# Kernel tuning notes

Measured on AMD Instinct MI355X. Metric: run time of the kernel, lower is better.

The kernel has to match this reference:

```python
import jax, jax.numpy as jnp
import numpy as np

K = 2  # top-k experts per token


def setup_inputs() -> dict:
    key = jax.random.key(0)
    ks = jax.random.split(key, 5)
    N, D, F, E = 8192, 1024, 1024, 8
    s = lambda d: 1.0 / np.sqrt(d)
    return {
        "x": jax.random.normal(ks[0], (N, D), jnp.float32),
        "Wr": jax.random.normal(ks[1], (D, E), jnp.float32) * s(D),
        "br": jax.random.normal(ks[2], (E,), jnp.float32) * 0.01,
        "We": jax.random.normal(ks[3], (E, D, F), jnp.float32) * s(D),
        "be": jax.random.normal(ks[4], (E, F), jnp.float32) * 0.01,
    }


def reference(x, Wr, br, We, be):
    # Router: logits [N, E] -> top-k -> softmax over the k selected logits
    logits = x @ Wr + br
    topv, idx = jax.lax.top_k(logits, K)            # [N, K]
    w = jax.nn.softmax(topv, axis=-1)               # [N, K]
    # All-expert dense compute (eval mode: dropout is identity)
    h = jnp.einsum("nd,edf->nef", x, We) + be       # [N, E, F]
    h = jax.nn.gelu(h, approximate=False)           # exact GELU (torch nn.GELU default)
    # Gather the k selected experts per token and combine
    sel = jnp.take_along_axis(h, idx[:, :, None], axis=1)  # [N, K, F]
    out = jnp.einsum("nk,nkf->nf", w, sel)          # [N, F]
    return out
```

## Files before the change

### kernel.cpp

```cpp
#include <hip/hip_runtime.h>
#include <hip/hip_bf16.h>
#include <math.h>
#include <stdint.h>

#define N_TOK 8192
#define DIM   1024
#define FDIM  1024
#define NEXP  8

typedef unsigned short u16;
typedef __bf16 bf16x8 __attribute__((ext_vector_type(8)));
typedef float  f32x4  __attribute__((ext_vector_type(4)));

__device__ __forceinline__ u16 f2bf(float f) {
  union { float f; uint32_t u; } v; v.f = f;
  return (u16)((v.u + 0x7fffu + ((v.u >> 16) & 1u)) >> 16);
}

__global__ __launch_bounds__(256) void k_prep(
    const float* __restrict__ x, const float* __restrict__ Wr,
    const float* __restrict__ br, const float* __restrict__ We,
    u16* __restrict__ xb, u16* __restrict__ WeT,
    int* __restrict__ topk_idx, float* __restrict__ topk_w0) {
  __shared__ float tile[64][65];
  int b = blockIdx.x;
  if (b < 2048) {
    int n = b * 4 + (threadIdx.x >> 6);
    int lane = threadIdx.x & 63;
    const float4* xr = (const float4*)(x + (size_t)n * DIM);
    ushort4* xbr = (ushort4*)(xb + (size_t)n * DIM);
    double acc[8];
#pragma unroll
    for (int e = 0; e < 8; ++e) acc[e] = 0.0;
#pragma unroll
    for (int i = 0; i < 4; ++i) {
      int d4 = lane + 64 * i;
      float4 v = xr[d4];
      ushort4 o;
      o.x = f2bf(v.x); o.y = f2bf(v.y); o.z = f2bf(v.z); o.w = f2bf(v.w);
      xbr[d4] = o;
      float vv[4] = {v.x, v.y, v.z, v.w};
      const float* wr = Wr + (size_t)d4 * 4 * NEXP;
#pragma unroll
      for (int j = 0; j < 4; ++j) {
        float4 w0 = *(const float4*)(wr + j * 8);
        float4 w1 = *(const float4*)(wr + j * 8 + 4);
        acc[0] += (double)vv[j] * w0.x; acc[1] += (double)vv[j] * w0.y;
        acc[2] += (double)vv[j] * w0.z; acc[3] += (double)vv[j] * w0.w;
        acc[4] += (double)vv[j] * w1.x; acc[5] += (double)vv[j] * w1.y;
        acc[6] += (double)vv[j] * w1.z; acc[7] += (double)vv[j] * w1.w;
      }
    }
#pragma unroll
    for (int e = 0; e < 8; ++e) {
      for (int off = 32; off; off >>= 1) acc[e] += __shfl_xor(acc[e], off);
    }
    if (lane == 0) {
      double lg[8];
#pragma unroll
      for (int e = 0; e < 8; ++e) lg[e] = acc[e] + (double)br[e];
      int i0 = 0; double v0 = lg[0];
#pragma unroll
      for (int e = 1; e < 8; ++e) if (lg[e] > v0) { v0 = lg[e]; i0 = e; }
      int i1 = -1; double v1 = -1e300;
#pragma unroll
      for (int e = 0; e < 8; ++e) if (e != i0 && lg[e] > v1) { v1 = lg[e]; i1 = e; }
      float w0 = 1.0f / (1.0f + expf((float)(v1 - v0)));
      topk_idx[n] = i0 | (i1 << 8);
      topk_w0[n] = w0;
    }
  } else {
    int tb = b - 2048;
    int e = tb >> 8;
    int d0 = ((tb >> 4) & 15) * 64, f0 = (tb & 15) * 64;
    int t = threadIdx.x;
    int lr = t >> 6, lc = t & 63;
    const float* src = We + (size_t)e * DIM * FDIM + (size_t)d0 * FDIM + f0;
#pragma unroll
    for (int i = 0; i < 16; ++i)
      tile[i * 4 + lr][lc] = src[(size_t)(i * 4 + lr) * FDIM + lc];
    __syncthreads();
    u16* dst = WeT + (size_t)e * FDIM * DIM + (size_t)f0 * DIM + d0;
#pragma unroll
    for (int i = 0; i < 16; ++i)
      dst[(size_t)(i * 4 + lr) * DIM + lc] = f2bf(tile[lc][i * 4 + lr]);
  }
}

__global__ __launch_bounds__(256) void k_build_lists(const int* __restrict__ topk_idx,
                                                     int* __restrict__ gcount,
                                                     int* __restrict__ token_list) {
  __shared__ int lcount[8];
  __shared__ int lbase[8];
  int t = threadIdx.x;
  int n = blockIdx.x * 256 + t;
  if (t < 8) lcount[t] = 0;
  __syncthreads();
  int pk = topk_idx[n];
  int e0 = pk & 0xff, e1 = (pk >> 8) & 0xff;
  int p0 = atomicAdd(&lcount[e0], 1);
  int p1 = atomicAdd(&lcount[e1], 1);
  __syncthreads();
  if (t < 8) lbase[t] = atomicAdd(&gcount[t], lcount[t]);
  __syncthreads();
  token_list[e0 * N_TOK + lbase[e0] + p0] = n * 2;
  token_list[e1 * N_TOK + lbase[e1] + p1] = n * 2 + 1;
}

#define BM 128
#define BN 128
#define BK 64
#define NWG 1088

__global__ __launch_bounds__(256, 2) void k_moe_gemm(
    const u16* __restrict__ xb, const u16* __restrict__ WeT,
    const int* __restrict__ gcount, const int* __restrict__ token_list,
    u16* __restrict__ hbuf) {
  int b = blockIdx.x;
  int w = (b & 7) * (NWG / 8) + (b >> 3);
  int e = -1, my = 0, fx = 0, cnt = 0, pfx = 0;
#pragma unroll
  for (int i = 0; i < NEXP; ++i) {
    int c = gcount[i];
    int tiles = ((c + BM - 1) >> 7) * (FDIM / BN);
    if (e < 0 && w < pfx + tiles) {
      e = i; int lw = w - pfx; my = lw >> 3; fx = lw & 7; cnt = c;
    }
    pfx += tiles;
  }
  if (e < 0) return;
  int m0 = my * BM, f0 = fx * BN;

  __shared__ u16 sA[BM * BK];
  __shared__ u16 sB[BN * BK];

  int tid = threadIdx.x;
  int lane = tid & 63, wid = tid >> 6;
  int wm = wid >> 1, wn = wid & 1;
  int rA = lane & 15, kg = lane >> 4;

  const int* tl = token_list + e * N_TOK;

  const u16* aA[4];
  const u16* aB[4];
  int cnt1 = cnt - 1;
#pragma unroll
  for (int it = 0; it < 4; ++it) {
    int c = it * 256 + tid;
    int row = c >> 3, cj = c & 7;
    int sw = (cj * 8) ^ ((row & 7) << 3);
    int slot = m0 + row; if (slot > cnt1) slot = cnt1;
    int tok = tl[slot] >> 1;
    aA[it] = xb + (size_t)tok * DIM + sw;
    aB[it] = WeT + ((size_t)(e * FDIM + f0 + row)) * DIM + sw;
  }

  f32x4 zero = {0.f, 0.f, 0.f, 0.f};
  f32x4 acc[4][4];
#pragma unroll
  for (int mi = 0; mi < 4; ++mi)
#pragma unroll
    for (int ni = 0; ni < 4; ++ni) acc[mi][ni] = zero;

  const char* pA = (const char*)sA + (wm * 64 + rA) * 128;
  const char* pB = (const char*)sB + (wn * 64 + rA) * 128;
  int swz = (rA & 7) << 4;

  for (int kt = 0; kt < DIM / BK; ++kt) {
    int k0 = kt * BK;
#pragma unroll
    for (int it = 0; it < 4; ++it) {
      __builtin_amdgcn_global_load_lds(
          (const __attribute__((address_space(1))) void*)(aA[it] + k0),
          (__attribute__((address_space(3))) void*)(sA + (it * 256 + tid) * 8), 16, 0, 0);
      __builtin_amdgcn_global_load_lds(
          (const __attribute__((address_space(1))) void*)(aB[it] + k0),
          (__attribute__((address_space(3))) void*)(sB + (it * 256 + tid) * 8), 16, 0, 0);
    }
    __syncthreads();
#pragma unroll
    for (int kk = 0; kk < 2; ++kk) {
      int kb = ((kk << 6) | (kg << 4)) ^ swz;
      bf16x8 av[4], bv[4];
#pragma unroll
      for (int mi = 0; mi < 4; ++mi)
        av[mi] = *(const bf16x8*)(pA + mi * 2048 + kb);
#pragma unroll
      for (int ni = 0; ni < 4; ++ni)
        bv[ni] = *(const bf16x8*)(pB + ni * 2048 + kb);
#pragma unroll
      for (int mi = 0; mi < 4; ++mi)
#pragma unroll
        for (int ni = 0; ni < 4; ++ni)
          acc[mi][ni] = __builtin_amdgcn_mfma_f32_16x16x32_bf16(av[mi], bv[ni], acc[mi][ni], 0, 0, 0);
    }
    __syncthreads();
  }

#pragma unroll
  for (int mi = 0; mi < 4; ++mi) {
#pragma unroll
    for (int j = 0; j < 4; ++j) {
      int slot = m0 + wm * 64 + mi * 16 + kg * 4 + j;
      if (slot < cnt) {
        int tok2 = tl[slot];
        u16* hrow = hbuf + (size_t)tok2 * FDIM;
        int colf = f0 + wn * 64 + rA;
#pragma unroll
        for (int ni = 0; ni < 4; ++ni)
          hrow[colf + ni * 16] = f2bf(acc[mi][ni][j]);
      }
    }
  }
}

__global__ __launch_bounds__(256) void k_combine(const u16* __restrict__ hbuf,
                                                 const int* __restrict__ topk_idx,
                                                 const float* __restrict__ topk_w0,
                                                 const float* __restrict__ be,
                                                 float* __restrict__ out) {
  int n = blockIdx.x * 2 + (threadIdx.x >> 7);
  int t = threadIdx.x & 127;
  int pk = topk_idx[n];
  int e0 = pk & 0xff, e1 = (pk >> 8) & 0xff;
  float w0 = topk_w0[n], w1 = 1.0f - w0;
  const bf16x8* r0 = (const bf16x8*)(hbuf + (size_t)(2 * n) * FDIM);
  const bf16x8* r1 = (const bf16x8*)(hbuf + (size_t)(2 * n + 1) * FDIM);
  bf16x8 a = r0[t], c = r1[t];
  const float* b0 = be + e0 * FDIM + t * 8;
  const float* b1 = be + e1 * FDIM + t * 8;
  float4 b0a = *(const float4*)(b0), b0b = *(const float4*)(b0 + 4);
  float4 b1a = *(const float4*)(b1), b1b = *(const float4*)(b1 + 4);
  float bb0[8] = {b0a.x, b0a.y, b0a.z, b0a.w, b0b.x, b0b.y, b0b.z, b0b.w};
  float bb1[8] = {b1a.x, b1a.y, b1a.z, b1a.w, b1b.x, b1b.y, b1b.z, b1b.w};
  float o[8];
#pragma unroll
  for (int i = 0; i < 8; ++i) {
    float v0 = (float)a[i] + bb0[i];
    float v1 = (float)c[i] + bb1[i];
    float g0 = 0.5f * v0 * (1.0f + erff(v0 * 0.70710678118654752f));
    float g1 = 0.5f * v1 * (1.0f + erff(v1 * 0.70710678118654752f));
    o[i] = w0 * g0 + w1 * g1;
  }
  float* orow = out + (size_t)n * FDIM + t * 8;
  *(float4*)(orow)     = *(float4*)(o);
  *(float4*)(orow + 4) = *(float4*)(o + 4);
}

extern "C" void kernel_launch(void* const* d_in, const int* in_sizes, int n_in,
                              void* d_out, int out_size, void* d_ws, size_t ws_size,
                              hipStream_t stream) {
  const float* x  = (const float*)d_in[0];
  const float* Wr = (const float*)d_in[1];
  const float* br = (const float*)d_in[2];
  const float* We = (const float*)d_in[3];
  const float* be = (const float*)d_in[4];
  float* out = (float*)d_out;

  char* ws = (char*)d_ws;
  u16* xb = (u16*)ws;                ws += (size_t)N_TOK * DIM * 2;
  u16* WeT = (u16*)ws;               ws += (size_t)NEXP * FDIM * DIM * 2;
  u16* hbuf = (u16*)ws;              ws += (size_t)2 * N_TOK * FDIM * 2;
  int* token_list = (int*)ws;        ws += (size_t)NEXP * N_TOK * 4;
  int* topk_idx = (int*)ws;          ws += (size_t)N_TOK * 4;
  float* topk_w0 = (float*)ws;       ws += (size_t)N_TOK * 4;
  int* gcount = (int*)ws;

  hipMemsetAsync(gcount, 0, NEXP * sizeof(int), stream);

  k_prep<<<dim3(4096), dim3(256), 0, stream>>>(x, Wr, br, We, xb, WeT, topk_idx, topk_w0);
  k_build_lists<<<dim3(N_TOK / 256), dim3(256), 0, stream>>>(topk_idx, gcount, token_list);
  k_moe_gemm<<<dim3(NWG), dim3(256), 0, stream>>>(xb, WeT, gcount, token_list, hbuf);
  k_combine<<<dim3(N_TOK / 2), dim3(256), 0, stream>>>(hbuf, topk_idx, topk_w0, be, out);
}
```

Measured before the change: 117.5 us.

## Double-buffer LDS tiles with BK=32 and prefetch next K-slice during MFMA

The expert GEMM's K tile shrinks from 64 to 32 and two LDS buffers are used, so the next K-slice's global-to-LDS loads are issued right after the barrier while MFMAs run on the current buffer. The global-load addressing and LDS swizzle are rebuilt for the 32-wide tile, with pairs of rows packed per 128-byte line. This drops one of the two barriers per iteration, aiming to hide global load latency behind compute. The trade-off is twice as many K iterations with less MFMA work between barriers, at the same total LDS footprint.

```diff
diff --git a/kernel.cpp b/kernel.cpp
--- a/kernel.cpp
+++ b/kernel.cpp
@@ -109,7 +109,8 @@
 
 #define BM 128
 #define BN 128
-#define BK 64
+#define BK 32
+#define NKT (DIM / BK)
 #define NWG 1088
 
 __global__ __launch_bounds__(256, 2) void k_moe_gemm(
@@ -131,8 +132,8 @@
   if (e < 0) return;
   int m0 = my * BM, f0 = fx * BN;
 
-  __shared__ u16 sA[BM * BK];
-  __shared__ u16 sB[BN * BK];
+  __shared__ u16 sA[2 * BM * BK];
+  __shared__ u16 sB[2 * BN * BK];
 
   int tid = threadIdx.x;
   int lane = tid & 63, wid = tid >> 6;
@@ -141,19 +142,34 @@
 
   const int* tl = token_list + e * N_TOK;
 
-  const u16* aA[4];
-  const u16* aB[4];
+  const u16* aA[2];
+  const u16* aB[2];
   int cnt1 = cnt - 1;
 #pragma unroll
-  for (int it = 0; it < 4; ++it) {
+  for (int it = 0; it < 2; ++it) {
     int c = it * 256 + tid;
-    int row = c >> 3, cj = c & 7;
-    int sw = (cj * 8) ^ ((row & 7) << 3);
+    int P = c >> 3, H = (c >> 2) & 1;
+    int k8 = (c & 3) ^ (P & 3);
+    int row = P * 2 + H;
     int slot = m0 + row; if (slot > cnt1) slot = cnt1;
     int tok = tl[slot] >> 1;
-    aA[it] = xb + (size_t)tok * DIM + sw;
-    aB[it] = WeT + ((size_t)(e * FDIM + f0 + row)) * DIM + sw;
-  }
+    aA[it] = xb + (size_t)tok * DIM + k8 * 8;
+    aB[it] = WeT + ((size_t)(e * FDIM + f0 + row)) * DIM + k8 * 8;
+  }
+
+  auto stage = [&](int buf, int k0) {
+#pragma unroll
+    for (int it = 0; it < 2; ++it) {
+      __builtin_amdgcn_global_load_lds(
+          (const __attribute__((address_space(1))) void*)(aA[it] + k0),
+          (__attribute__((address_space(3))) void*)(sA + buf * (BM * BK) + (it * 256 + tid) * 8),
+          16, 0, 0);
+      __builtin_amdgcn_global_load_lds(
+          (const __attribute__((address_space(1))) void*)(aB[it] + k0),
+          (__attribute__((address_space(3))) void*)(sB + buf * (BN * BK) + (it * 256 + tid) * 8),
+          16, 0, 0);
+    }
+  };
 
   f32x4 zero = {0.f, 0.f, 0.f, 0.f};
   f32x4 acc[4][4];
@@ -162,39 +178,32 @@
 #pragma unroll
     for (int ni = 0; ni < 4; ++ni) acc[mi][ni] = zero;
 
-  const char* pA = (const char*)sA + (wm * 64 + rA) * 128;
-  const char* pB = (const char*)sB + (wn * 64 + rA) * 128;
-  int swz = (rA & 7) << 4;
-
-  for (int kt = 0; kt < DIM / BK; ++kt) {
-    int k0 = kt * BK;
-#pragma unroll
-    for (int it = 0; it < 4; ++it) {
-      __builtin_amdgcn_global_load_lds(
-          (const __attribute__((address_space(1))) void*)(aA[it] + k0),
-          (__attribute__((address_space(3))) void*)(sA + (it * 256 + tid) * 8), 16, 0, 0);
-      __builtin_amdgcn_global_load_lds(
-          (const __attribute__((address_space(1))) void*)(aB[it] + k0),
-          (__attribute__((address_space(3))) void*)(sB + (it * 256 + tid) * 8), 16, 0, 0);
-    }
+  int lanebase = (rA >> 1) * 128 + (rA & 1) * 64 + ((kg << 4) ^ (((rA >> 1) & 3) << 4));
+  const char* pA = (const char*)sA + wm * 4096 + lanebase;
+  const char* pB = (const char*)sB + wn * 4096 + lanebase;
+
+  stage(0, 0);
+  int buf = 0;
+  for (int kt = 0; kt < NKT; ++kt) {
     __syncthreads();
-#pragma unroll
-    for (int kk = 0; kk < 2; ++kk) {
-      int kb = ((kk << 6) | (kg << 4)) ^ swz;
+    if (kt + 1 < NKT) stage(buf ^ 1, (kt + 1) * BK);
+    {
+      const char* qA = pA + buf * (BM * BK * 2);
+      const char* qB = pB + buf * (BN * BK * 2);
       bf16x8 av[4], bv[4];
 #pragma unroll
       for (int mi = 0; mi < 4; ++mi)
-        av[mi] = *(const bf16x8*)(pA + mi * 2048 + kb);
+        av[mi] = *(const bf16x8*)(qA + mi * 1024);
 #pragma unroll
       for (int ni = 0; ni < 4; ++ni)
-        bv[ni] = *(const bf16x8*)(pB + ni * 2048 + kb);
+        bv[ni] = *(const bf16x8*)(qB + ni * 1024);
 #pragma unroll
       for (int mi = 0; mi < 4; ++mi)
 #pragma unroll
         for (int ni = 0; ni < 4; ++ni)
           acc[mi][ni] = __builtin_amdgcn_mfma_f32_16x16x32_bf16(av[mi], bv[ni], acc[mi][ni], 0, 0, 0);
     }
-    __syncthreads();
+    buf ^= 1;
   }
 
 #pragma unroll
```

New measurement: 126.0 us. +7.2%, slower.
